# Kernel tuning notes

Measured on AMD Instinct MI355X. Metric: run time of the kernel, lower is better.

## Reference

```python
import jax, jax.numpy as jnp
import numpy as np

B, H, S, D = 1, 16, 4096, 64
TEMPERATURE = 8.0          # sqrt(d_k)
WINDOW_SIZE = 256
HALF_WINDOW = WINDOW_SIZE // 2
NEG_INF = -1000000000.0


def setup_inputs() -> dict:
    key = jax.random.key(0)
    kq, kk, kv = jax.random.split(key, 3)
    q = jax.random.normal(kq, (B, H, S, D), dtype=jnp.float32)
    k = jax.random.normal(kk, (B, H, S, D), dtype=jnp.float32)
    v = jax.random.normal(kv, (B, H, S, D), dtype=jnp.float32)
    return {"q": q, "k": k, "v": v}


def reference(q, k, v):
    # q,k,v: [B,H,S,D]
    seq = q.shape[2]
    attn = jnp.einsum('bhqd,bhkd->bhqk', q, k) / TEMPERATURE  # [B,H,S,S]
    if seq > WINDOW_SIZE:
        idx = jnp.arange(seq)
        # torch loop: row i allows columns [i-half, i+half] inclusive
        win = jnp.abs(idx[:, None] - idx[None, :]) <= HALF_WINDOW  # [S,S]
        attn = jnp.where(win[None, None, :, :], attn, NEG_INF)
    attn = jax.nn.softmax(attn, axis=-1)  # dropout p=0 -> identity
    out = jnp.einsum('bhqk,bhkd->bhqd', attn, v)
    return (out, attn)
```

## Files before the change

### kernel.cpp

```cpp
#include <hip/hip_runtime.h>
#include <hip/hip_bf16.h>


typedef short bf16x8 __attribute__((ext_vector_type(8)));
typedef float f32x4  __attribute__((ext_vector_type(4)));
typedef unsigned int u32;
typedef unsigned short u16;

namespace {
constexpr int S = 4096, H = 16, Dh = 64, TR = 16, HW = 128, NCH = 5;
constexpr int UW  = NCH * 64;
constexpr int PBW = UW + 8;
}

__device__ __forceinline__ u16 f2bf(float x) {
    u32 u = __float_as_uint(x);
    return (u16)((u + 0x7fffu + ((u >> 16) & 1u)) >> 16);
}
__device__ __forceinline__ float bf2f(u16 h) {
    return __uint_as_float(((u32)h) << 16);
}

__global__ __launch_bounds__(256)
void prep(const float* __restrict__ k, const float* __restrict__ v,
          u16* __restrict__ k_hi, u16* __restrict__ k_lo, u16* __restrict__ v_t)
{
    __shared__ u16 vt[Dh * 65];
    const int tid = threadIdx.x;
    const int h  = blockIdx.x >> 6;
    const int s0 = (blockIdx.x & 63) * 64;
    const int r = tid >> 2, dseg = (tid & 3) * 16;

    {
        const float* src = k + ((size_t)(h * S + s0 + r) * Dh + dseg);
        u16 hi[16] __attribute__((aligned(16)));
        u16 lo[16] __attribute__((aligned(16)));
        #pragma unroll
        for (int i4 = 0; i4 < 4; ++i4) {
            float4 t = *(const float4*)(src + i4 * 4);
            float xs[4] = {t.x, t.y, t.z, t.w};
            #pragma unroll
            for (int i = 0; i < 4; ++i) {
                u16 hh = f2bf(xs[i]);
                hi[i4 * 4 + i] = hh;
                lo[i4 * 4 + i] = f2bf(xs[i] - bf2f(hh));
            }
        }
        const size_t o = (size_t)(h * S + s0 + r) * Dh + dseg;
        *(int4*)(k_hi + o)     = *(const int4*)(hi);
        *(int4*)(k_hi + o + 8) = *(const int4*)(hi + 8);
        *(int4*)(k_lo + o)     = *(const int4*)(lo);
        *(int4*)(k_lo + o + 8) = *(const int4*)(lo + 8);
    }
    {
        const float* src = v + ((size_t)(h * S + s0 + r) * Dh + dseg);
        #pragma unroll
        for (int i4 = 0; i4 < 4; ++i4) {
            float4 t = *(const float4*)(src + i4 * 4);
            float xs[4] = {t.x, t.y, t.z, t.w};
            #pragma unroll
            for (int i = 0; i < 4; ++i)
                vt[(dseg + i4 * 4 + i) * 65 + r] = f2bf(xs[i]);
        }
    }
    __syncthreads();
    {
        const int d = tid >> 2, rseg = (tid & 3) * 16;
        u16 tmp[16] __attribute__((aligned(16)));
        #pragma unroll
        for (int i = 0; i < 16; ++i) tmp[i] = vt[d * 65 + rseg + i];
        const size_t o = (size_t)(h * Dh + d) * S + s0 + rseg;
        *(int4*)(v_t + o)     = *(const int4*)(tmp);
        *(int4*)(v_t + o + 8) = *(const int4*)(tmp + 8);
    }
}

__global__ __launch_bounds__(256, 4)
void wattn(const float* __restrict__ q,
           const u16* __restrict__ k_hi, const u16* __restrict__ k_lo,
           const u16* __restrict__ v_t,
           float* __restrict__ out, float* __restrict__ attn)
{
    __shared__ __align__(16) u16 pb_[TR * PBW];
    __shared__ float red[TR * 4];
    __shared__ float inv_row[TR];

    const int tid = threadIdx.x;
    const int wave = tid >> 6, lane = tid & 63;
    const int g = lane >> 4, m = lane & 15;

    int bx = blockIdx.x;
    bx = (bx & 7) * (H * (S / TR) / 8) + (bx >> 3);
    const int h  = bx >> 8;
    const int r0 = (bx & 255) * TR;
    const int c0 = max(0, r0 - HW);
    const int c1 = min(S - 1, r0 + TR - 1 + HW);

    bf16x8 aqh[2], aql[2];
    {
        const float* qrow = q + (size_t)(h * S + r0 + m) * Dh + g * 8;
        #pragma unroll
        for (int ks = 0; ks < 2; ++ks) {
            float4 t0 = *(const float4*)(qrow + ks * 32);
            float4 t1 = *(const float4*)(qrow + ks * 32 + 4);
            float xs[8] = {t0.x, t0.y, t0.z, t0.w, t1.x, t1.y, t1.z, t1.w};
            #pragma unroll
            for (int i = 0; i < 8; ++i) {
                u16 hh = f2bf(xs[i]);
                aqh[ks][i] = (short)hh;
                aql[ks][i] = (short)f2bf(xs[i] - bf2f(hh));
            }
        }
    }

    f32x4 sc[NCH];
    #pragma unroll
    for (int cc = 0; cc < NCH; ++cc) {
        const int col = min(c0 + cc * 64 + wave * 16 + m, S - 1);
        const u16* ph = k_hi + (size_t)(h * S + col) * Dh + g * 8;
        const u16* pl = k_lo + (size_t)(h * S + col) * Dh + g * 8;
        f32x4 acc = {0.f, 0.f, 0.f, 0.f};
        #pragma unroll
        for (int ks = 0; ks < 2; ++ks) {
            bf16x8 bh = *(const bf16x8*)(ph + ks * 32);
            bf16x8 bl = *(const bf16x8*)(pl + ks * 32);
            acc = __builtin_amdgcn_mfma_f32_16x16x32_bf16(aqh[ks], bh, acc, 0, 0, 0);
            acc = __builtin_amdgcn_mfma_f32_16x16x32_bf16(aql[ks], bh, acc, 0, 0, 0);
            acc = __builtin_amdgcn_mfma_f32_16x16x32_bf16(aqh[ks], bl, acc, 0, 0, 0);
        }
        sc[cc] = acc;
    }

    float rs[4] = {0.f, 0.f, 0.f, 0.f};
    #pragma unroll
    for (int cc = 0; cc < NCH; ++cc) {
        const int colg = c0 + cc * 64 + wave * 16 + m;
        #pragma unroll
        for (int w = 0; w < 4; ++w) {
            const int row = r0 + g * 4 + w;
            const bool ok = (colg >= row - HW) && (colg <= row + HW) && (colg <= c1);
            const float ev = ok ? __expf(sc[cc][w] * 0.125f) : 0.f;
            rs[w] += ev;
            pb_[(g * 4 + w) * PBW + cc * 64 + wave * 16 + m] = f2bf(ev);
        }
    }
    #pragma unroll
    for (int off = 1; off < 16; off <<= 1) {
        #pragma unroll
        for (int w = 0; w < 4; ++w) rs[w] += __shfl_xor(rs[w], off, 64);
    }
    if (m == 0) {
        #pragma unroll
        for (int w = 0; w < 4; ++w) red[(g * 4 + w) * 4 + wave] = rs[w];
    }
    __syncthreads();
    if (tid < TR) {
        float4 p4 = *(const float4*)(red + tid * 4);
        inv_row[tid] = 1.0f / (p4.x + p4.y + p4.z + p4.w);
    }
    __syncthreads();

    f32x4 oacc = {0.f, 0.f, 0.f, 0.f};
    {
        const u16* vrow = v_t + (size_t)(h * Dh + wave * 16 + m) * S;
        #pragma unroll
        for (int cc = 0; cc < NCH; ++cc) {
            #pragma unroll
            for (int ks = 0; ks < 2; ++ks) {
                const int j = min(c0 + cc * 64 + ks * 32 + g * 8, S - 8);
                bf16x8 ap = *(const bf16x8*)(pb_ + m * PBW + cc * 64 + ks * 32 + g * 8);
                bf16x8 bv = *(const bf16x8*)(vrow + j);
                oacc = __builtin_amdgcn_mfma_f32_16x16x32_bf16(ap, bv, oacc, 0, 0, 0);
            }
        }
    }
    {
        float* op = out + (size_t)(h * S + r0 + g * 4) * Dh + wave * 16 + m;
        #pragma unroll
        for (int w = 0; w < 4; ++w)
            op[(size_t)w * Dh] = oacc[w] * inv_row[g * 4 + w];
    }

    {
        float* arow = attn + ((size_t)(h * S + r0)) * S;
        const int c0q = c0 >> 2;
        for (int r = 0; r < TR; ++r) {
            const float inv = inv_row[r];
            float4* dst = (float4*)(arow + (size_t)r * S);
            #pragma unroll
            for (int kk = 0; kk < 4; ++kk) {
                const int c4 = tid + 256 * kk;
                const int o4 = c4 - c0q;
                float4 val = {0.f, 0.f, 0.f, 0.f};
                if ((unsigned)o4 < (unsigned)(UW / 4)) {
                    ushort4 hh = *(const ushort4*)(pb_ + r * PBW + o4 * 4);
                    val.x = bf2f(hh.x) * inv; val.y = bf2f(hh.y) * inv;
                    val.z = bf2f(hh.z) * inv; val.w = bf2f(hh.w) * inv;
                }
                dst[c4] = val;
            }
        }
    }
}

extern "C" void kernel_launch(void* const* d_in, const int* in_sizes, int n_in,
                              void* d_out, int out_size, void* d_ws, size_t ws_size,
                              hipStream_t stream) {
    const float* q = (const float*)d_in[0];
    const float* k = (const float*)d_in[1];
    const float* v = (const float*)d_in[2];
    float* out  = (float*)d_out;
    float* attn = out + (size_t)H * S * Dh;
    u16* k_hi = (u16*)d_ws;
    u16* k_lo = k_hi + (size_t)H * S * Dh;
    u16* v_t  = k_lo + (size_t)H * S * Dh;
    prep <<<dim3(H * (S / 64)), dim3(256), 0, stream>>>(k, v, k_hi, k_lo, v_t);
    wattn<<<dim3(H * (S / TR)), dim3(256), 0, stream>>>(q, k_hi, k_lo, v_t, out, attn);
}
```

Measured before the change: 1.107 ms.

## Split zero-fill of attention matrix into separate kernel, write only band in wattn

Adds a zfill kernel that writes zeros to every attention element outside each row-tile's band window. The wattn kernel now writes only the banded window values, with a flat index over 16 rows × UQ float4s, and does so before the PV MFMA stage rather than after. The aim is to separate the bulk zero stream from the compute kernel so that kernel stays short and its stores are compact. Total bytes written are the same, and one extra kernel launch is added.

```diff
diff --git a/kernel.cpp b/kernel.cpp
--- a/kernel.cpp
+++ b/kernel.cpp
@@ -10,6 +10,7 @@
 namespace {
 constexpr int S = 4096, H = 16, Dh = 64, TR = 16, HW = 128, NCH = 5;
 constexpr int UW  = NCH * 64;
+constexpr int UQ  = UW / 4;
 constexpr int PBW = UW + 8;
 }
 
@@ -19,6 +20,22 @@
 }
 __device__ __forceinline__ float bf2f(u16 h) {
     return __uint_as_float(((u32)h) << 16);
+}
+
+__global__ __launch_bounds__(256)
+void zfill(float4* __restrict__ attn4)
+{
+    const int tid = blockIdx.x * 256 + threadIdx.x;
+    #pragma unroll
+    for (int i = 0; i < 16; ++i) {
+        const int f  = tid + i * 4194304;
+        const int r  = (f >> 10) & (S - 1);
+        const int r0 = r & ~(TR - 1);
+        const int c0q = max(0, r0 - HW) >> 2;
+        const int o4  = f & 1023;
+        if (o4 < c0q || o4 >= c0q + UQ)
+            attn4[f] = make_float4(0.f, 0.f, 0.f, 0.f);
+    }
 }
 
 __global__ __launch_bounds__(256)
@@ -160,6 +177,25 @@
     }
     __syncthreads();
 
+    {
+        float* arow = attn + ((size_t)(h * S + r0)) * S;
+        const int c0q = c0 >> 2;
+        #pragma unroll
+        for (int it = 0; it < 5; ++it) {
+            const int idx = tid + 256 * it;
+            const int r   = idx / UQ;
+            const int o4  = idx - r * UQ;
+            const int c4  = c0q + o4;
+            if (c4 < S / 4) {
+                ushort4 hh = *(const ushort4*)(pb_ + r * PBW + o4 * 4);
+                const float inv = inv_row[r];
+                float4 val = {bf2f(hh.x) * inv, bf2f(hh.y) * inv,
+                              bf2f(hh.z) * inv, bf2f(hh.w) * inv};
+                *(float4*)(arow + (size_t)r * S + c4 * 4) = val;
+            }
+        }
+    }
+
     f32x4 oacc = {0.f, 0.f, 0.f, 0.f};
     {
         const u16* vrow = v_t + (size_t)(h * Dh + wave * 16 + m) * S;
@@ -179,27 +215,6 @@
         #pragma unroll
         for (int w = 0; w < 4; ++w)
             op[(size_t)w * Dh] = oacc[w] * inv_row[g * 4 + w];
-    }
-
-    {
-        float* arow = attn + ((size_t)(h * S + r0)) * S;
-        const int c0q = c0 >> 2;
-        for (int r = 0; r < TR; ++r) {
-            const float inv = inv_row[r];
-            float4* dst = (float4*)(arow + (size_t)r * S);
-            #pragma unroll
-            for (int kk = 0; kk < 4; ++kk) {
-                const int c4 = tid + 256 * kk;
-                const int o4 = c4 - c0q;
-                float4 val = {0.f, 0.f, 0.f, 0.f};
-                if ((unsigned)o4 < (unsigned)(UW / 4)) {
-                    ushort4 hh = *(const ushort4*)(pb_ + r * PBW + o4 * 4);
-                    val.x = bf2f(hh.x) * inv; val.y = bf2f(hh.y) * inv;
-                    val.z = bf2f(hh.z) * inv; val.w = bf2f(hh.w) * inv;
-                }
-                dst[c4] = val;
-            }
-        }
     }
 }
 
@@ -214,6 +229,7 @@
     u16* k_hi = (u16*)d_ws;
     u16* k_lo = k_hi + (size_t)H * S * Dh;
     u16* v_t  = k_lo + (size_t)H * S * Dh;
-    prep <<<dim3(H * (S / 64)), dim3(256), 0, stream>>>(k, v, k_hi, k_lo, v_t);
-    wattn<<<dim3(H * (S / TR)), dim3(256), 0, stream>>>(q, k_hi, k_lo, v_t, out, attn);
-}
+    zfill<<<dim3(16384),          dim3(256), 0, stream>>>((float4*)attn);
+    prep <<<dim3(H * (S / 64)),   dim3(256), 0, stream>>>(k, v, k_hi, k_lo, v_t);
+    wattn<<<dim3(H * (S / TR)),   dim3(256), 0, stream>>>(q, k_hi, k_lo, v_t, out, attn);
+}
```

Result: slower. 1.191 ms (+7.6%).

## Store normalized fp32 probabilities in LDS and split attn writes with nontemporal stores

Applied to the files above, without the earlier changes.

The probabilities are normalized in registers and staged as fp32 in shared memory instead of unnormalized bf16. The window band is written from that buffer, and the zero region outside the band is written separately, both with nontemporal stores. The attention matrix therefore keeps full fp32 precision rather than a bf16-rounded copy. The cost is a larger LDS footprint, an extra barrier, and converting fp32 to bf16 per element for the PV MFMA. Because the probabilities are already normalized, the output scaling step goes away.

```diff
diff --git a/kernel.cpp b/kernel.cpp
--- a/kernel.cpp
+++ b/kernel.cpp
@@ -9,8 +9,9 @@
 
 namespace {
 constexpr int S = 4096, H = 16, Dh = 64, TR = 16, HW = 128, NCH = 5;
-constexpr int UW  = NCH * 64;
-constexpr int PBW = UW + 8;
+constexpr int UW = NCH * 64;
+constexpr int UQ = UW / 4;
+constexpr int PF = 324;
 }
 
 __device__ __forceinline__ u16 f2bf(float x) {
@@ -81,7 +82,7 @@
            const u16* __restrict__ v_t,
            float* __restrict__ out, float* __restrict__ attn)
 {
-    __shared__ __align__(16) u16 pb_[TR * PBW];
+    __shared__ __align__(16) float pf[TR * PF];
     __shared__ float red[TR * 4];
     __shared__ float inv_row[TR];
 
@@ -95,6 +96,7 @@
     const int r0 = (bx & 255) * TR;
     const int c0 = max(0, r0 - HW);
     const int c1 = min(S - 1, r0 + TR - 1 + HW);
+    const int c0q = c0 >> 2;
 
     bf16x8 aqh[2], aql[2];
     {
@@ -140,8 +142,8 @@
             const int row = r0 + g * 4 + w;
             const bool ok = (colg >= row - HW) && (colg <= row + HW) && (colg <= c1);
             const float ev = ok ? __expf(sc[cc][w] * 0.125f) : 0.f;
+            sc[cc][w] = ev;
             rs[w] += ev;
-            pb_[(g * 4 + w) * PBW + cc * 64 + wave * 16 + m] = f2bf(ev);
         }
     }
     #pragma unroll
@@ -160,6 +162,30 @@
     }
     __syncthreads();
 
+    #pragma unroll
+    for (int w = 0; w < 4; ++w) {
+        const float inv = inv_row[g * 4 + w];
+        #pragma unroll
+        for (int cc = 0; cc < NCH; ++cc)
+            pf[(g * 4 + w) * PF + cc * 64 + wave * 16 + m] = sc[cc][w] * inv;
+    }
+    __syncthreads();
+
+    float* arow = attn + ((size_t)(h * S + r0)) * S;
+
+    {
+        const int r = tid >> 4, t16 = tid & 15;
+        #pragma unroll
+        for (int it = 0; it < 5; ++it) {
+            const int o4 = t16 + (it << 4);
+            const int c4 = c0q + o4;
+            if (c4 < S / 4) {
+                f32x4 val = *(const f32x4*)(pf + r * PF + (o4 << 2));
+                __builtin_nontemporal_store(val, (f32x4*)(arow + ((size_t)r << 12) + (c4 << 2)));
+            }
+        }
+    }
+
     f32x4 oacc = {0.f, 0.f, 0.f, 0.f};
     {
         const u16* vrow = v_t + (size_t)(h * Dh + wave * 16 + m) * S;
@@ -168,7 +194,10 @@
             #pragma unroll
             for (int ks = 0; ks < 2; ++ks) {
                 const int j = min(c0 + cc * 64 + ks * 32 + g * 8, S - 8);
-                bf16x8 ap = *(const bf16x8*)(pb_ + m * PBW + cc * 64 + ks * 32 + g * 8);
+                const float* pp = pf + m * PF + cc * 64 + ks * 32 + g * 8;
+                bf16x8 ap;
+                #pragma unroll
+                for (int i = 0; i < 8; ++i) ap[i] = (short)f2bf(pp[i]);
                 bf16x8 bv = *(const bf16x8*)(vrow + j);
                 oacc = __builtin_amdgcn_mfma_f32_16x16x32_bf16(ap, bv, oacc, 0, 0, 0);
             }
@@ -178,27 +207,18 @@
         float* op = out + (size_t)(h * S + r0 + g * 4) * Dh + wave * 16 + m;
         #pragma unroll
         for (int w = 0; w < 4; ++w)
-            op[(size_t)w * Dh] = oacc[w] * inv_row[g * 4 + w];
-    }
-
-    {
-        float* arow = attn + ((size_t)(h * S + r0)) * S;
-        const int c0q = c0 >> 2;
-        for (int r = 0; r < TR; ++r) {
-            const float inv = inv_row[r];
-            float4* dst = (float4*)(arow + (size_t)r * S);
-            #pragma unroll
-            for (int kk = 0; kk < 4; ++kk) {
-                const int c4 = tid + 256 * kk;
-                const int o4 = c4 - c0q;
-                float4 val = {0.f, 0.f, 0.f, 0.f};
-                if ((unsigned)o4 < (unsigned)(UW / 4)) {
-                    ushort4 hh = *(const ushort4*)(pb_ + r * PBW + o4 * 4);
-                    val.x = bf2f(hh.x) * inv; val.y = bf2f(hh.y) * inv;
-                    val.z = bf2f(hh.z) * inv; val.w = bf2f(hh.w) * inv;
-                }
-                dst[c4] = val;
-            }
+            op[(size_t)w * Dh] = oacc[w];
+    }
+
+    {
+        const f32x4 z4 = {0.f, 0.f, 0.f, 0.f};
+        #pragma unroll 8
+        for (int it = 0; it < 64; ++it) {
+            const int idx = tid + (it << 8);
+            const int row = idx >> 10;
+            const int c4  = idx & 1023;
+            if ((u32)(c4 - c0q) >= (u32)UQ)
+                __builtin_nontemporal_store(z4, (f32x4*)(arow + ((size_t)row << 12) + (c4 << 2)));
         }
     }
 }
```

Result: no change. 1.109 ms (+0.1%).
